# Optimization experiments

Hardware: AMD Instinct MI355X
Metric: run time of the kernel (lower is better)

The kernel has to match this reference:

```python
import jax, jax.numpy as jnp
import numpy as np

B, S, H = 4, 2048, 1024
NH, HD = 8, 128  # num_heads, head_dim

def setup_inputs() -> dict:
    key = jax.random.key(0)
    ks = jax.random.split(key, 5)
    scale = 1.0 / np.sqrt(H)
    return {
        "hidden_states": jax.random.normal(ks[0], (B, S, H), dtype=jnp.float32),
        "Wq": jax.random.normal(ks[1], (H, H), dtype=jnp.float32) * scale,
        "Wk": jax.random.normal(ks[2], (H, H), dtype=jnp.float32) * scale,
        "Wv": jax.random.normal(ks[3], (H, H), dtype=jnp.float32) * scale,
        "Wo": jax.random.normal(ks[4], (H, H), dtype=jnp.float32) * scale,
    }

def reference(hidden_states, Wq, Wk, Wv, Wo):
    # projections (torch Linear: x @ W.T), weights stored [out, in]
    q = hidden_states @ Wq.T
    k = hidden_states @ Wk.T
    v = hidden_states @ Wv.T
    # [B, NH, S, HD]
    q = q.reshape(B, S, NH, HD).transpose(0, 2, 1, 3)
    k = k.reshape(B, S, NH, HD).transpose(0, 2, 1, 3)
    v = v.reshape(B, S, NH, HD).transpose(0, 2, 1, 3)
    scale = 1.0 / jnp.sqrt(jnp.asarray(HD, dtype=q.dtype))
    scores = jnp.einsum("bhqd,bhkd->bhqk", q, k) * scale
    # softmax in fp32, cast back to input dtype (matches torch F.softmax dtype=float32)
    attn = jax.nn.softmax(scores.astype(jnp.float32), axis=-1).astype(q.dtype)
    out = jnp.einsum("bhqk,bhkd->bhqd", attn, v)
    out = out.transpose(0, 2, 1, 3).reshape(B, S, H)
    return out @ Wo.T
```

## Files before the change

kernel.cpp:

```cpp
#include <hip/hip_runtime.h>
#include <stdint.h>

#define Bz  4
#define Sz  2048
#define Hz  1024
#define NHz 8
#define HDz 128
#define Mz  (Bz*Sz)

typedef __attribute__((ext_vector_type(8))) short bf16x8;
typedef __attribute__((ext_vector_type(4))) float f32x4;
typedef __attribute__((ext_vector_type(16))) float f32x16;

__device__ __forceinline__ unsigned short f2bf(float x) {
  union { float f; unsigned int u; } c; c.f = x;
  unsigned int u = c.u;
  return (unsigned short)((u + 0x7FFFu + ((u >> 16) & 1u)) >> 16);
}

__device__ __forceinline__ unsigned cvtpk(float lo, float hi_) {
  unsigned r;
  asm("v_cvt_pk_bf16_f32 %0, %1, %2" : "=v"(r) : "v"(lo), "v"(hi_));
  return r;
}

__device__ __forceinline__ void gl2lds16(const unsigned short* g, unsigned short* l) {
  __builtin_amdgcn_global_load_lds(
      (const __attribute__((address_space(1))) unsigned int*)g,
      (__attribute__((address_space(3))) unsigned int*)l, 16, 0, 0);
}

__global__ __launch_bounds__(256)
void cvt_kernel(const float* __restrict__ in, unsigned short* __restrict__ out, int n) {
  const int n4 = n >> 2;
  for (int i = blockIdx.x * blockDim.x + threadIdx.x; i < n4; i += gridDim.x * blockDim.x) {
    float4 v = ((const float4*)in)[i];
    ushort4 o;
    o.x = f2bf(v.x); o.y = f2bf(v.y); o.z = f2bf(v.z); o.w = f2bf(v.w);
    ((ushort4*)out)[i] = o;
  }
}

__global__ __launch_bounds__(256)
void cvt4_kernel(const float* __restrict__ w0, const float* __restrict__ w1,
                 const float* __restrict__ w2, const float* __restrict__ w3,
                 unsigned short* __restrict__ o0, unsigned short* __restrict__ o1,
                 unsigned short* __restrict__ o2, unsigned short* __restrict__ o3) {
  const int which = blockIdx.y;
  const float* in = (which == 0) ? w0 : (which == 1) ? w1 : (which == 2) ? w2 : w3;
  unsigned short* out = (which == 0) ? o0 : (which == 1) ? o1 : (which == 2) ? o2 : o3;
  const int n4 = (Hz * Hz) >> 2;
  for (int i = blockIdx.x * blockDim.x + threadIdx.x; i < n4; i += gridDim.x * blockDim.x) {
    float4 v = ((const float4*)in)[i];
    ushort4 o;
    o.x = f2bf(v.x); o.y = f2bf(v.y); o.z = f2bf(v.z); o.w = f2bf(v.w);
    ((ushort4*)out)[i] = o;
  }
}

#define GEMM_PROLOG()                                                           \
  __shared__ __align__(16) unsigned short Asm[128 * 64];                        \
  __shared__ __align__(16) unsigned short Bsm[128 * 64];                        \
  const int tid = threadIdx.x;                                                  \
  const int w  = tid >> 6, l = tid & 63;                                        \
  const int lc = l & 15,  lg = l >> 4;                                          \
  const int wr = w >> 1,  wc = w & 1;                                           \
  const int bm = blockIdx.x * 128;                                              \
  const int bn = blockIdx.y * 128;                                              \
  f32x4 acc[4][4];                                                              \
  _Pragma("unroll")                                                             \
  for (int i = 0; i < 4; i++)                                                   \
    _Pragma("unroll")                                                           \
    for (int j = 0; j < 4; j++) acc[i][j] = (f32x4){0.f, 0.f, 0.f, 0.f};        \
  const int srow = w * 32 + (l >> 3);                                           \
  const int scol = (l & 7) * 8;                                                 \
  for (int kt = 0; kt < 16; kt++) {                                             \
    const int k0 = kt * 64;                                                     \
    __syncthreads();                                                            \
    _Pragma("unroll")                                                           \
    for (int i = 0; i < 4; i++) {                                               \
      gl2lds16(A  + (size_t)(bm + srow + i * 8) * Hz + k0 + scol,               \
               &Asm[(w * 32 + i * 8) * 64]);                                    \
      gl2lds16(Bw + (size_t)(bn + srow + i * 8) * Hz + k0 + scol,               \
               &Bsm[(w * 32 + i * 8) * 64]);                                    \
    }                                                                           \
    __syncthreads();                                                            \
    _Pragma("unroll")                                                           \
    for (int kk = 0; kk < 2; kk++) {                                            \
      bf16x8 af[4], bf[4];                                                      \
      _Pragma("unroll")                                                         \
      for (int t = 0; t < 4; t++) {                                             \
        af[t] = *(const bf16x8*)&Asm[(wr*64 + t*16 + lc)*64 + kk*32 + lg*8];    \
        bf[t] = *(const bf16x8*)&Bsm[(wc*64 + t*16 + lc)*64 + kk*32 + lg*8];    \
      }                                                                         \
      _Pragma("unroll")                                                         \
      for (int mt = 0; mt < 4; mt++)                                            \
        _Pragma("unroll")                                                       \
        for (int nt = 0; nt < 4; nt++)                                          \
          acc[mt][nt] = __builtin_amdgcn_mfma_f32_16x16x32_bf16(                \
              af[mt], bf[nt], acc[mt][nt], 0, 0, 0);                            \
    }                                                                           \
  }

__global__ __launch_bounds__(256)
void gemm_qkv(const unsigned short* __restrict__ A,
              const unsigned short* __restrict__ W0,
              const unsigned short* __restrict__ W1,
              const unsigned short* __restrict__ W2,
              unsigned short* __restrict__ Qo,
              unsigned short* __restrict__ Ko,
              unsigned short* __restrict__ Vto, float qscale)
{
  const int z = blockIdx.z;
  const unsigned short* Bw = (z == 0) ? W0 : (z == 1) ? W1 : W2;
  const float alpha = (z == 0) ? qscale : 1.0f;
  GEMM_PROLOG()

#pragma unroll
  for (int mt = 0; mt < 4; mt++) {
#pragma unroll
    for (int nt = 0; nt < 4; nt++) {
      const int row0 = bm + wr * 64 + mt * 16 + lg * 4;
      const int col  = bn + wc * 64 + nt * 16 + lc;
      if (z == 2) {
        ushort4 pk;
        pk.x = f2bf(acc[mt][nt][0]);
        pk.y = f2bf(acc[mt][nt][1]);
        pk.z = f2bf(acc[mt][nt][2]);
        pk.w = f2bf(acc[mt][nt][3]);
        const size_t idx = ((size_t)((row0 >> 11) << 10) + col) * Sz + (row0 & 2047);
        *(ushort4*)&Vto[idx] = pk;
      } else {
        unsigned short* C = (z == 0) ? Qo : Ko;
#pragma unroll
        for (int r = 0; r < 4; r++)
          C[(size_t)(row0 + r) * Hz + col] = f2bf(acc[mt][nt][r] * alpha);
      }
    }
  }
}

__global__ __launch_bounds__(256)
void gemm_out(const unsigned short* __restrict__ A,
              const unsigned short* __restrict__ Bw,
              float* __restrict__ C)
{
  GEMM_PROLOG()
#pragma unroll
  for (int mt = 0; mt < 4; mt++)
#pragma unroll
    for (int nt = 0; nt < 4; nt++) {
      const int row0 = bm + wr * 64 + mt * 16 + lg * 4;
      const int col  = bn + wc * 64 + nt * 16 + lc;
#pragma unroll
      for (int r = 0; r < 4; r++)
        C[(size_t)(row0 + r) * Hz + col] = acc[mt][nt][r];
    }
}

__global__ __launch_bounds__(256, 2)
void attn_fwd(const unsigned short* __restrict__ Q,
              const unsigned short* __restrict__ K,
              const unsigned short* __restrict__ Vt,
              unsigned short* __restrict__ O)
{
  const int bid = blockIdx.x;
  const int wg  = (bid & 7) * 64 + (bid >> 3);
  const int qb  = wg & 15;
  const int bh  = wg >> 4;
  const int b = bh >> 3, nh = bh & 7;
  const int w = threadIdx.x >> 6, l = threadIdx.x & 63;
  const int l31 = l & 31, hi = l >> 5;

  __shared__ __align__(16) unsigned short Ksm[2][64 * 128];
  __shared__ __align__(16) unsigned short Vsm[128 * 64];

  bf16x8 qf[8];
#pragma unroll
  for (int ks = 0; ks < 8; ks++)
    qf[ks] = *(const bf16x8*)(Q + ((size_t)b * Sz + qb * 128 + w * 32 + l31) * Hz
                                + nh * HDz + ks * 16 + hi * 8);

  const unsigned short* Kbase = K  + (size_t)b * Sz * Hz + nh * HDz;
  const unsigned short* Vbase = Vt + (size_t)bh * HDz * Sz;

  f32x16 acc[4];
#pragma unroll
  for (int d = 0; d < 4; d++)
#pragma unroll
    for (int i = 0; i < 16; i++) acc[d][i] = 0.f;
  float mrow = -3.0e38f, lrowp = 0.f;

  union PA { unsigned wd[4]; bf16x8 v; };

  #define STAGE_K(BUF, KT) {                                                          \
    _Pragma("unroll")                                                                 \
    for (int i = 0; i < 4; i++) {                                                     \
      const int r = w * 16 + i * 4 + (l >> 4);                                        \
      gl2lds16(Kbase + (size_t)((KT) * 64 + r) * Hz + (((l & 15) ^ (r & 7)) * 8),     \
               &Ksm[BUF][(w * 16 + i * 4) * 128]);                                    \
    } }
  #define STAGE_V(KT) {                                                               \
    _Pragma("unroll")                                                                 \
    for (int i = 0; i < 4; i++) {                                                     \
      const int r = w * 32 + i * 8 + (l >> 3);                                        \
      gl2lds16(Vbase + (size_t)r * Sz + (KT) * 64 + (((l & 7) ^ (r & 7)) * 8),        \
               &Vsm[(w * 32 + i * 8) * 64]);                                          \
    } }

  int cur = 0;
  STAGE_K(0, 0);
  __syncthreads();

  for (int kt = 0; kt < Sz / 64; kt++) {
    STAGE_V(kt);
    if (kt < Sz / 64 - 1) STAGE_K(cur ^ 1, kt + 1);

    f32x16 st[2];
#pragma unroll
    for (int i = 0; i < 16; i++) { st[0][i] = 0.f; st[1][i] = 0.f; }
#pragma unroll
    for (int ks = 0; ks < 8; ks++) {
      bf16x8 kf0 = *(const bf16x8*)&Ksm[cur][(l31) * 128 + (((ks * 2 + hi) ^ (l31 & 7)) * 8)];
      st[0] = __builtin_amdgcn_mfma_f32_32x32x16_bf16(kf0, qf[ks], st[0], 0, 0, 0);
      bf16x8 kf1 = *(const bf16x8*)&Ksm[cur][(32 + l31) * 128 + (((ks * 2 + hi) ^ (l31 & 7)) * 8)];
      st[1] = __builtin_amdgcn_mfma_f32_32x32x16_bf16(kf1, qf[ks], st[1], 0, 0, 0);
    }

    float t16[16];
#pragma unroll
    for (int i = 0; i < 16; i++) t16[i] = fmaxf(st[0][i], st[1][i]);
#pragma unroll
    for (int s = 8; s > 0; s >>= 1)
#pragma unroll
      for (int i = 0; i < s; i++) t16[i] = fmaxf(t16[i], t16[i + s]);
    const float tm = fmaxf(t16[0], __shfl_xor(t16[0], 32));

    float sc = 1.0f;
    const bool trig = tm > mrow + 8.0f;
    if (trig) { sc = exp2f(mrow - tm); mrow = tm; lrowp *= sc; }
    if (__any(trig)) {
#pragma unroll
      for (int r = 0; r < 16; r++) {
        const float scr = __shfl(sc, (r & 3) + 8 * (r >> 2) + 4 * hi);
#pragma unroll
        for (int d = 0; d < 4; d++) acc[d][r] *= scr;
      }
    }

    float ps = 0.f;
#pragma unroll
    for (int n = 0; n < 2; n++)
#pragma unroll
      for (int i = 0; i < 16; i++) {
        const float p = exp2f(st[n][i] - mrow);
        st[n][i] = p;
        ps += p;
      }
    lrowp += ps;

    PA pa[4];
#pragma unroll
    for (int n = 0; n < 2; n++) {
      unsigned Wp[8];
#pragma unroll
      for (int m = 0; m < 4; m++) {
        Wp[m * 2 + 0] = cvtpk(st[n][4 * m + 0], st[n][4 * m + 1]);
        Wp[m * 2 + 1] = cvtpk(st[n][4 * m + 2], st[n][4 * m + 3]);
      }
#pragma unroll
      for (int ks2 = 0; ks2 < 2; ks2++) {
#pragma unroll
        for (int h = 0; h < 2; h++) {
          const unsigned a0 = Wp[(2 * ks2) * 2 + h];
          const unsigned a1 = Wp[(2 * ks2 + 1) * 2 + h];
          const unsigned own  = hi ? a1 : a0;
          const unsigned send = hi ? a0 : a1;
          const unsigned part = __shfl_xor(send, 32);
          pa[n * 2 + ks2].wd[0 + h] = hi ? part : own;
          pa[n * 2 + ks2].wd[2 + h] = hi ? own : part;
        }
      }
    }

    __syncthreads();

#pragma unroll
    for (int t = 0; t < 4; t++)
#pragma unroll
      for (int d = 0; d < 4; d++) {
        bf16x8 vf = *(const bf16x8*)&Vsm[(d * 32 + l31) * 64 + (((t * 2 + hi) ^ (l31 & 7)) * 8)];
        acc[d] = __builtin_amdgcn_mfma_f32_32x32x16_bf16(pa[t].v, vf, acc[d], 0, 0, 0);
      }

    __syncthreads();
    cur ^= 1;
  }

  const float lsum = lrowp + __shfl_xor(lrowp, 32);
  const float inv = 1.0f / lsum;
#pragma unroll
  for (int r = 0; r < 16; r++) {
    const float ir = __shfl(inv, (r & 3) + 8 * (r >> 2) + 4 * hi);
    const size_t row = (size_t)b * Sz + qb * 128 + w * 32 + (r & 3) + 8 * (r >> 2) + 4 * hi;
#pragma unroll
    for (int d = 0; d < 4; d++)
      O[row * Hz + nh * HDz + d * 32 + l31] = f2bf(acc[d][r] * ir);
  }
}

extern "C" void kernel_launch(void* const* d_in, const int* in_sizes, int n_in,
                              void* d_out, int out_size, void* d_ws, size_t ws_size,
                              hipStream_t stream) {
  const float* hs = (const float*)d_in[0];
  const float* Wq = (const float*)d_in[1];
  const float* Wk = (const float*)d_in[2];
  const float* Wv = (const float*)d_in[3];
  const float* Wo = (const float*)d_in[4];

  const size_t NEL = (size_t)Mz * Hz;
  const size_t WEL = (size_t)Hz * Hz;

  unsigned short* p = (unsigned short*)d_ws;
  unsigned short* hs_bf = p; p += NEL;
  unsigned short* Wq_bf = p; p += WEL;
  unsigned short* Wk_bf = p; p += WEL;
  unsigned short* Wv_bf = p; p += WEL;
  unsigned short* Wo_bf = p; p += WEL;
  unsigned short* Qb    = p; p += NEL;
  unsigned short* Kb    = p; p += NEL;
  unsigned short* Vtb   = p; p += NEL;
  unsigned short* Ob    = hs_bf;

  cvt_kernel<<<2048, 256, 0, stream>>>(hs, hs_bf, (int)NEL);
  cvt4_kernel<<<dim3(512, 4), 256, 0, stream>>>(Wq, Wk, Wv, Wo,
                                                Wq_bf, Wk_bf, Wv_bf, Wo_bf);

  const float qscale = 0.08838834764831845f * 1.44269504088896340736f;
  gemm_qkv<<<dim3(Mz / 128, Hz / 128, 3), 256, 0, stream>>>(
      hs_bf, Wq_bf, Wk_bf, Wv_bf, Qb, Kb, Vtb, qscale);

  attn_fwd<<<512, 256, 0, stream>>>(Qb, Kb, Vtb, Ob);

  gemm_out<<<dim3(Mz / 128, Hz / 128), 256, 0, stream>>>(Ob, Wo_bf, (float*)d_out);
}
```

Before: 295.8 us.

## Load V fragments directly to registers, set MFMA priority, merge convert kernels

The attention kernel no longer stages V tiles in LDS. Each lane loads its V^T fragments straight from global memory into 16 registers at the start of each key tile, which removes one barrier per iteration and halves LDS use. MFMA sections are wrapped in s_setprio to favour matrix issue across waves, and the two fp32-to-bf16 conversion launches are merged into one 5-slice grid. The risks are higher register pressure that may hurt 2-waves-per-SIMD occupancy, uncoalesced strided global reads for V, and fewer blocks for the large hidden-state conversion slice.

```diff
diff --git a/kernel.cpp b/kernel.cpp
--- a/kernel.cpp
+++ b/kernel.cpp
@@ -31,25 +31,16 @@
 }
 
 __global__ __launch_bounds__(256)
-void cvt_kernel(const float* __restrict__ in, unsigned short* __restrict__ out, int n) {
-  const int n4 = n >> 2;
-  for (int i = blockIdx.x * blockDim.x + threadIdx.x; i < n4; i += gridDim.x * blockDim.x) {
-    float4 v = ((const float4*)in)[i];
-    ushort4 o;
-    o.x = f2bf(v.x); o.y = f2bf(v.y); o.z = f2bf(v.z); o.w = f2bf(v.w);
-    ((ushort4*)out)[i] = o;
-  }
-}
-
-__global__ __launch_bounds__(256)
-void cvt4_kernel(const float* __restrict__ w0, const float* __restrict__ w1,
-                 const float* __restrict__ w2, const float* __restrict__ w3,
-                 unsigned short* __restrict__ o0, unsigned short* __restrict__ o1,
-                 unsigned short* __restrict__ o2, unsigned short* __restrict__ o3) {
-  const int which = blockIdx.y;
-  const float* in = (which == 0) ? w0 : (which == 1) ? w1 : (which == 2) ? w2 : w3;
-  unsigned short* out = (which == 0) ? o0 : (which == 1) ? o1 : (which == 2) ? o2 : o3;
-  const int n4 = (Hz * Hz) >> 2;
+void cvt_all(const float* __restrict__ hs,
+             const float* __restrict__ w0, const float* __restrict__ w1,
+             const float* __restrict__ w2, const float* __restrict__ w3,
+             unsigned short* __restrict__ ohs,
+             unsigned short* __restrict__ o0, unsigned short* __restrict__ o1,
+             unsigned short* __restrict__ o2, unsigned short* __restrict__ o3) {
+  const int y = blockIdx.y;
+  const float* in = (y == 0) ? hs : (y == 1) ? w0 : (y == 2) ? w1 : (y == 3) ? w2 : w3;
+  unsigned short* out = (y == 0) ? ohs : (y == 1) ? o0 : (y == 2) ? o1 : (y == 3) ? o2 : o3;
+  const int n4 = ((y == 0) ? (Mz * Hz) : (Hz * Hz)) >> 2;
   for (int i = blockIdx.x * blockDim.x + threadIdx.x; i < n4; i += gridDim.x * blockDim.x) {
     float4 v = ((const float4*)in)[i];
     ushort4 o;
@@ -173,7 +164,6 @@
   const int l31 = l & 31, hi = l >> 5;
 
   __shared__ __align__(16) unsigned short Ksm[2][64 * 128];
-  __shared__ __align__(16) unsigned short Vsm[128 * 64];
 
   bf16x8 qf[8];
 #pragma unroll
@@ -182,7 +172,7 @@
                                 + nh * HDz + ks * 16 + hi * 8);
 
   const unsigned short* Kbase = K  + (size_t)b * Sz * Hz + nh * HDz;
-  const unsigned short* Vbase = Vt + (size_t)bh * HDz * Sz;
+  const unsigned short* Vl = Vt + (size_t)bh * HDz * Sz + (size_t)l31 * Sz + hi * 8;
 
   f32x16 acc[4];
 #pragma unroll
@@ -200,25 +190,24 @@
       gl2lds16(Kbase + (size_t)((KT) * 64 + r) * Hz + (((l & 15) ^ (r & 7)) * 8),     \
                &Ksm[BUF][(w * 16 + i * 4) * 128]);                                    \
     } }
-  #define STAGE_V(KT) {                                                               \
-    _Pragma("unroll")                                                                 \
-    for (int i = 0; i < 4; i++) {                                                     \
-      const int r = w * 32 + i * 8 + (l >> 3);                                        \
-      gl2lds16(Vbase + (size_t)r * Sz + (KT) * 64 + (((l & 7) ^ (r & 7)) * 8),        \
-               &Vsm[(w * 32 + i * 8) * 64]);                                          \
-    } }
 
   int cur = 0;
   STAGE_K(0, 0);
   __syncthreads();
 
   for (int kt = 0; kt < Sz / 64; kt++) {
-    STAGE_V(kt);
     if (kt < Sz / 64 - 1) STAGE_K(cur ^ 1, kt + 1);
+    bf16x8 vfr[16];
+#pragma unroll
+    for (int t = 0; t < 4; t++)
+#pragma unroll
+      for (int d = 0; d < 4; d++)
+        vfr[t * 4 + d] = *(const bf16x8*)(Vl + (size_t)(d * 32) * Sz + kt * 64 + t * 16);
 
     f32x16 st[2];
 #pragma unroll
     for (int i = 0; i < 16; i++) { st[0][i] = 0.f; st[1][i] = 0.f; }
+    __builtin_amdgcn_s_setprio(1);
 #pragma unroll
     for (int ks = 0; ks < 8; ks++) {
       bf16x8 kf0 = *(const bf16x8*)&Ksm[cur][(l31) * 128 + (((ks * 2 + hi) ^ (l31 & 7)) * 8)];
@@ -226,6 +215,7 @@
       bf16x8 kf1 = *(const bf16x8*)&Ksm[cur][(32 + l31) * 128 + (((ks * 2 + hi) ^ (l31 & 7)) * 8)];
       st[1] = __builtin_amdgcn_mfma_f32_32x32x16_bf16(kf1, qf[ks], st[1], 0, 0, 0);
     }
+    __builtin_amdgcn_s_setprio(0);
 
     float t16[16];
 #pragma unroll
@@ -283,15 +273,13 @@
       }
     }
 
-    __syncthreads();
-
+    __builtin_amdgcn_s_setprio(1);
 #pragma unroll
     for (int t = 0; t < 4; t++)
 #pragma unroll
-      for (int d = 0; d < 4; d++) {
-        bf16x8 vf = *(const bf16x8*)&Vsm[(d * 32 + l31) * 64 + (((t * 2 + hi) ^ (l31 & 7)) * 8)];
-        acc[d] = __builtin_amdgcn_mfma_f32_32x32x16_bf16(pa[t].v, vf, acc[d], 0, 0, 0);
-      }
+      for (int d = 0; d < 4; d++)
+        acc[d] = __builtin_amdgcn_mfma_f32_32x32x16_bf16(pa[t].v, vfr[t * 4 + d], acc[d], 0, 0, 0);
+    __builtin_amdgcn_s_setprio(0);
 
     __syncthreads();
     cur ^= 1;
@@ -332,9 +320,8 @@
   unsigned short* Vtb   = p; p += NEL;
   unsigned short* Ob    = hs_bf;
 
-  cvt_kernel<<<2048, 256, 0, stream>>>(hs, hs_bf, (int)NEL);
-  cvt4_kernel<<<dim3(512, 4), 256, 0, stream>>>(Wq, Wk, Wv, Wo,
-                                                Wq_bf, Wk_bf, Wv_bf, Wo_bf);
+  cvt_all<<<dim3(512, 5), 256, 0, stream>>>(hs, Wq, Wk, Wv, Wo,
+                                            hs_bf, Wq_bf, Wk_bf, Wv_bf, Wo_bf);
 
   const float qscale = 0.08838834764831845f * 1.44269504088896340736f;
   gemm_qkv<<<dim3(Mz / 128, Hz / 128, 3), 256, 0, stream>>>(
```

Result: slower. 345.3 us (+16.7%).
